# Kernel tuning notes

Hardware: AMD Instinct MI355X
Metric: run time of the kernel (lower is better)

The kernel has to match this reference:

```python
import jax, jax.numpy as jnp
import numpy as np

N, P, Q, H_DIM, HEADS, D = 4096, 128, 128, 256, 8, 64  # D = graph_dim // heads


def setup_inputs() -> dict:
    key = jax.random.key(0)
    ks = jax.random.split(key, 6)
    s = 0.05  # small scale to keep tanh/softmax in a sane range
    return {
        "x_prices": jax.random.normal(ks[0], (N, P), jnp.float32),
        "x_news": jax.random.normal(ks[1], (N, Q), jnp.float32),
        "W_bil": jax.random.normal(ks[2], (H_DIM, P, Q), jnp.float32) * s,
        "b_bil": jax.random.normal(ks[3], (H_DIM,), jnp.float32) * s,
        "Wt": jax.random.normal(ks[4], (HEADS, D, H_DIM), jnp.float32) * s,
        "a_vec": jax.random.normal(ks[5], (HEADS, 2 * D), jnp.float32) * s,
    }


def reference(x_prices, x_news, W_bil, b_bil, Wt, a_vec):
    # nn.Bilinear: out[n,h] = sum_pq x_prices[n,p] W[h,p,q] x_news[n,q] + b[h]
    x = jnp.einsum('np,hpq,nq->nh', x_prices, W_bil, x_news) + b_bil  # (N, hidden)

    # Per-head linear transform: fc_transform (no bias). Wt: (heads, d, hidden)
    xt = jnp.einsum('nh,kdh->knd', x, Wt)  # (heads, N, d)

    # Attention score a . [x_i, x_j] split into src/dst halves -> broadcast add
    d = Wt.shape[1]
    a_src, a_dst = a_vec[:, :d], a_vec[:, d:]
    s_src = jnp.einsum('knd,kd->kn', xt, a_src)  # (heads, N)
    s_dst = jnp.einsum('knd,kd->kn', xt, a_dst)  # (heads, N)
    scores = s_src[:, :, None] + s_dst[:, None, :]  # (heads, N, N)
    scores = jnp.where(scores >= 0, scores, 0.2 * scores)  # LeakyReLU(0.2)

    attn = jax.nn.softmax(scores, axis=-1)  # softmax over neighbors j
    out = jnp.einsum('knm,kmd->knd', attn, xt)  # (heads, N, d)

    # Concatenate head outputs on feature dim, then tanh
    out = jnp.transpose(out, (1, 0, 2)).reshape(xt.shape[1], -1)  # (N, heads*d)
    return jnp.tanh(out)
```

## Files before the change

kernel.cpp:

```cpp
#include <hip/hip_runtime.h>
#include <hip/hip_bf16.h>

typedef unsigned short ushort;
typedef unsigned int uint;
typedef unsigned long long u64;
typedef _Float16 f16;

#define NN 4096
#define PP 128
#define QQ 128
#define HD 256
#define KH 8
#define DD 64
#define KK 16384

typedef _Float16 f16x2 __attribute__((ext_vector_type(2)));
typedef _Float16 f16x4 __attribute__((ext_vector_type(4)));
typedef _Float16 f16x8 __attribute__((ext_vector_type(8)));
typedef __fp16 fp16x2 __attribute__((ext_vector_type(2)));
typedef float f32x4 __attribute__((ext_vector_type(4)));

__device__ inline void async_lds16(const void* g, void* l) {
  __builtin_amdgcn_global_load_lds(
      (const __attribute__((address_space(1))) unsigned int*)g,
      (__attribute__((address_space(3))) unsigned int*)l, 16, 0, 0);
}

__global__ __launch_bounds__(256) void k0_split2(
    const float* __restrict__ W, const float* __restrict__ Wt,
    f16* __restrict__ hiW, f16* __restrict__ loW,
    f16* __restrict__ hiT, f16* __restrict__ loT, float* __restrict__ xz) {
  const int tid = blockIdx.x * 256 + threadIdx.x;
  const int i = tid * 4;
  if (tid < (NN * HD) / 4)
    *(float4*)&xz[i] = make_float4(0.f, 0.f, 0.f, 0.f);
  const float* src;
  f16 *hi, *lo;
  int off;
  if (i < HD * PP * QQ) { src = W; hi = hiW; lo = loW; off = i; }
  else { src = Wt; hi = hiT; lo = loT; off = i - HD * PP * QQ; }
  const float4 w = *(const float4*)&src[off];
  const float wf[4] = {w.x, w.y, w.z, w.w};
  f16x4 hv, lv;
#pragma unroll
  for (int j = 0; j < 4; ++j) {
    const f16 h = (f16)wf[j];
    hv[j] = h;
    lv[j] = (f16)(wf[j] - (float)h);
  }
  *(f16x4*)&hi[off] = hv;
  *(f16x4*)&lo[off] = lv;
}

__global__ __launch_bounds__(256, 3) void k1_bilinear(
    const float* __restrict__ xp, const float* __restrict__ xn,
    const f16* __restrict__ Whi, const f16* __restrict__ Wlo,
    float* __restrict__ xout) {
  __shared__ f16 whi[2][128 * 32];
  __shared__ f16 wlo[2][128 * 32];
  __shared__ f16 zhi[128 * 40];
  __shared__ float xpt[8][128];

  const int t = threadIdx.x;
  const int n0 = blockIdx.x * 128;
  const int kb = blockIdx.y * (KK / 16);
  const int h0 = blockIdx.z * 128;
  const int pb = kb >> 7;

  const int l = t & 63, w = t >> 6;
  const int wr = (w >> 1) * 64, wc = (w & 1) * 64;

  int aoff[4], boff[4];
#pragma unroll
  for (int i = 0; i < 4; ++i)
    aoff[i] = (wr + i * 16 + (l & 15)) * 40 + (l >> 4) * 8;
#pragma unroll
  for (int j = 0; j < 4; ++j) {
    const int hr = wc + j * 16 + (l & 15);
    boff[j] = hr * 32 + (((l >> 4) ^ ((hr ^ (hr >> 2)) & 3)) * 8);
  }

  const int shb = t >> 2, seg = t & 3;
  int gsw[2];
#pragma unroll
  for (int g = 0; g < 2; ++g) {
    const int r = shb + 64 * g;
    gsw[g] = seg ^ ((r ^ (r >> 2)) & 3);
  }

  for (int idx = t; idx < 1024; idx += 256) {
    const int p = idx & 7, n = idx >> 3;
    xpt[p][n] = xp[(size_t)(n0 + n) * PP + pb + p];
  }

  auto stage_w = [&](int buf, int kc_) {
#pragma unroll
    for (int g = 0; g < 2; ++g) {
      const int r = shb + 64 * g;
      async_lds16(Whi + (size_t)(h0 + r) * KK + kc_ + gsw[g] * 8,
                  &whi[buf][r * 32 + seg * 8]);
      async_lds16(Wlo + (size_t)(h0 + r) * KK + kc_ + gsw[g] * 8,
                  &wlo[buf][r * 32 + seg * 8]);
    }
  };

  stage_w(0, kb);

  const int zn = t >> 1, zko = (t & 1) * 16;

  f32x4 acc[4][4];
#pragma unroll
  for (int i = 0; i < 4; ++i)
#pragma unroll
    for (int j = 0; j < 4; ++j) acc[i][j] = (f32x4)0.f;

  for (int c = 0; c < 32; ++c) {
    const int kc = kb + c * 32;
    const int pl = c >> 2;
    const int q0 = (c & 3) * 32;
    const int cur = c & 1, nxt = cur ^ 1;

    asm volatile("s_waitcnt lgkmcnt(0)" ::: "memory");
    __builtin_amdgcn_s_barrier();

    const float* xr = xn + (size_t)(n0 + zn) * QQ + q0 + zko;
    const float4 v0 = ((const float4*)xr)[0];
    const float4 v1 = ((const float4*)xr)[1];
    const float4 v2 = ((const float4*)xr)[2];
    const float4 v3 = ((const float4*)xr)[3];
    __builtin_amdgcn_sched_barrier(0);

    if (c < 31) stage_w(nxt, kc + 32);

    {
      const float xpv = xpt[pl][zn];
      float zz[16] = {v0.x, v0.y, v0.z, v0.w, v1.x, v1.y, v1.z, v1.w,
                      v2.x, v2.y, v2.z, v2.w, v3.x, v3.y, v3.z, v3.w};
      union { uint u[8]; uint4 q[2]; } ph;
#pragma unroll
      for (int j = 0; j < 8; ++j) {
        union { fp16x2 h; uint u; } cv;
        cv.h = __builtin_amdgcn_cvt_pkrtz(xpv * zz[2 * j], xpv * zz[2 * j + 1]);
        ph.u[j] = cv.u;
      }
      const int zo = zn * 40 + zko;
      *(uint4*)&zhi[zo] = ph.q[0];
      *(uint4*)&zhi[zo + 8] = ph.q[1];
    }

    if (c < 31)
      asm volatile("s_waitcnt vmcnt(4) lgkmcnt(0)" ::: "memory");
    else
      asm volatile("s_waitcnt vmcnt(0) lgkmcnt(0)" ::: "memory");
    __builtin_amdgcn_s_barrier();

    f16x8 Ah[4];
#pragma unroll
    for (int i = 0; i < 4; ++i) Ah[i] = *(const f16x8*)&zhi[aoff[i]];
#pragma unroll
    for (int j = 0; j < 4; ++j) {
      const f16x8 Bh = *(const f16x8*)&whi[cur][boff[j]];
      const f16x8 Bl = *(const f16x8*)&wlo[cur][boff[j]];
#pragma unroll
      for (int i = 0; i < 4; ++i)
        acc[i][j] = __builtin_amdgcn_mfma_f32_16x16x32_f16(Ah[i], Bh, acc[i][j], 0, 0, 0);
#pragma unroll
      for (int i = 0; i < 4; ++i)
        acc[i][j] = __builtin_amdgcn_mfma_f32_16x16x32_f16(Ah[i], Bl, acc[i][j], 0, 0, 0);
    }
  }

#pragma unroll
  for (int i = 0; i < 4; ++i)
#pragma unroll
    for (int j = 0; j < 4; ++j) {
      const int row = n0 + wr + i * 16 + (l >> 4) * 4;
      const int col = h0 + wc + j * 16 + (l & 15);
#pragma unroll
      for (int r = 0; r < 4; ++r)
        atomicAdd(&xout[(size_t)(row + r) * HD + col], acc[i][j][r]);
    }
}

__global__ __launch_bounds__(256) void k23_xt(
    const float* __restrict__ x, const float* __restrict__ bb,
    const f16* __restrict__ Wthi, const f16* __restrict__ Wtlo,
    const float* __restrict__ av, float* __restrict__ xt,
    float* __restrict__ ssrc, float* __restrict__ sdst) {
  __shared__ f16 ah[64 * 40];
  __shared__ f16 bh[128 * 32];
  __shared__ f16 bl[128 * 32];
  __shared__ float red1[2][64][17];
  __shared__ float red2[2][64][17];
  const int t = threadIdx.x;
  const int n0 = blockIdx.x * 64;
  const int c0 = blockIdx.y * 128;
  const int l = t & 63, w = t >> 6;
  const int wn = (w & 1) * 32, wcc = (w >> 1) * 64;

  int aoff[2], boff[4];
#pragma unroll
  for (int i = 0; i < 2; ++i)
    aoff[i] = (wn + i * 16 + (l & 15)) * 40 + (l >> 4) * 8;
#pragma unroll
  for (int j = 0; j < 4; ++j) {
    const int hr = wcc + j * 16 + (l & 15);
    boff[j] = hr * 32 + (((l >> 4) ^ ((hr ^ (hr >> 2)) & 3)) * 8);
  }

  f32x4 acc[2][4];
#pragma unroll
  for (int i = 0; i < 2; ++i)
#pragma unroll
    for (int j = 0; j < 4; ++j) acc[i][j] = (f32x4)0.f;

  for (int kc = 0; kc < HD; kc += 32) {
    __syncthreads();
    {
      const int row = t >> 2, sg = t & 3;
      const float* xr = &x[(size_t)(n0 + row) * HD + kc + sg * 8];
      const float4 xa = ((const float4*)xr)[0];
      const float4 xb = ((const float4*)xr)[1];
      const float4 ba = *(const float4*)&bb[kc + sg * 8];
      const float4 bv = *(const float4*)&bb[kc + sg * 8 + 4];
      f16x8 o;
      o[0] = (f16)(xa.x + ba.x); o[1] = (f16)(xa.y + ba.y);
      o[2] = (f16)(xa.z + ba.z); o[3] = (f16)(xa.w + ba.w);
      o[4] = (f16)(xb.x + bv.x); o[5] = (f16)(xb.y + bv.y);
      o[6] = (f16)(xb.z + bv.z); o[7] = (f16)(xb.w + bv.w);
      *(f16x8*)&ah[row * 40 + sg * 8] = o;
    }
#pragma unroll
    for (int g = 0; g < 2; ++g) {
      const int slot = g * 256 + t;
      const int col = slot >> 2, ps = slot & 3;
      const int ls = ps ^ ((col ^ (col >> 2)) & 3);
      *(uint4*)&bh[col * 32 + ps * 8] =
          *(const uint4*)&Wthi[(size_t)(c0 + col) * HD + kc + ls * 8];
      *(uint4*)&bl[col * 32 + ps * 8] =
          *(const uint4*)&Wtlo[(size_t)(c0 + col) * HD + kc + ls * 8];
    }
    __syncthreads();
    f16x8 Af[2];
#pragma unroll
    for (int i = 0; i < 2; ++i) Af[i] = *(const f16x8*)&ah[aoff[i]];
#pragma unroll
    for (int j = 0; j < 4; ++j) {
      const f16x8 Bh = *(const f16x8*)&bh[boff[j]];
      const f16x8 Bl = *(const f16x8*)&bl[boff[j]];
#pragma unroll
      for (int i = 0; i < 2; ++i)
        acc[i][j] = __builtin_amdgcn_mfma_f32_16x16x32_f16(Af[i], Bh, acc[i][j], 0, 0, 0);
#pragma unroll
      for (int i = 0; i < 2; ++i)
        acc[i][j] = __builtin_amdgcn_mfma_f32_16x16x32_f16(Af[i], Bl, acc[i][j], 0, 0, 0);
    }
  }

  const int hh = w >> 1;
  const int khead = (c0 >> 6) + hh;
  float a1v[4], a2v[4];
#pragma unroll
  for (int j = 0; j < 4; ++j) {
    const int d = j * 16 + (l & 15);
    a1v[j] = av[khead * (2 * DD) + d];
    a2v[j] = av[khead * (2 * DD) + DD + d];
  }

#pragma unroll
  for (int i = 0; i < 2; ++i)
#pragma unroll
    for (int r = 0; r < 4; ++r) {
      const int rowl = wn + i * 16 + (l >> 4) * 4 + r;
      float p1 = 0.f, p2 = 0.f;
#pragma unroll
      for (int j = 0; j < 4; ++j) {
        p1 += acc[i][j][r] * a1v[j];
        p2 += acc[i][j][r] * a2v[j];
      }
      red1[hh][rowl][l & 15] = p1;
      red2[hh][rowl][l & 15] = p2;
    }

#pragma unroll
  for (int i = 0; i < 2; ++i)
#pragma unroll
    for (int j = 0; j < 4; ++j) {
      const int row = n0 + wn + i * 16 + (l >> 4) * 4;
      const int colg = c0 + wcc + j * 16 + (l & 15);
      const int k = colg >> 6, d = colg & 63;
#pragma unroll
      for (int r = 0; r < 4; ++r)
        xt[((size_t)(k * NN + row + r)) * DD + d] = acc[i][j][r];
    }

  __syncthreads();
  {
    const int hh2 = t >> 7;
    const int which = (t >> 6) & 1;
    const int row = t & 63;
    const float* rp = which ? &red2[hh2][row][0] : &red1[hh2][row][0];
    float s = 0.f;
#pragma unroll
    for (int g = 0; g < 16; ++g) s += rp[g];
    const int kk = (c0 >> 6) + hh2;
    if (which) sdst[kk * NN + n0 + row] = s;
    else ssrc[kk * NN + n0 + row] = s;
  }
}

__global__ __launch_bounds__(256) void k4_rank(
    const float* __restrict__ sdst, float* __restrict__ vsorted,
    int* __restrict__ perm) {
  __shared__ u64 kv[4096];
  const int k = blockIdx.y, t = threadIdx.x;
  for (int i = t; i < 4096; i += 256) {
    const uint u = __float_as_uint(sdst[k * NN + i]);
    const uint key = (u & 0x80000000u) ? ~u : (u | 0x80000000u);
    kv[i] = ((u64)key << 32) | (uint)i;
  }
  __syncthreads();
  const int m = blockIdx.x * 256 + t;
  const u64 my = kv[m];
  int cnt = 0;
#pragma unroll 16
  for (int j = 0; j < 4096; ++j) cnt += (kv[j] < my) ? 1 : 0;
  const uint key = (uint)(my >> 32);
  const uint u = (key & 0x80000000u) ? (key ^ 0x80000000u) : ~key;
  vsorted[k * NN + cnt] = __uint_as_float(u);
  perm[k * NN + cnt] = (int)(my & 0xFFFFFFFFu);
}

__global__ __launch_bounds__(64) void k4b_chunksum(
    const float* __restrict__ vs, const int* __restrict__ perm,
    const float* __restrict__ xt, float* __restrict__ Chi, float* __restrict__ Clo) {
  __shared__ float rows[64][64];
  __shared__ float eh[64], el[64];
  const int c = blockIdx.x, k = blockIdx.y, t = threadIdx.x;
  const int base = k * NN + c * 64;
  {
    const float v = vs[base + t];
    eh[t] = __expf(v);
    el[t] = __expf(0.2f * v);
  }
#pragma unroll
  for (int r = 0; r < 16; ++r) {
    const int i = r * 4 + (t >> 4);
    const int p = perm[base + i];
    *(float4*)&rows[i][(t & 15) * 4] =
        *(const float4*)&xt[((size_t)(k * NN + p)) * DD + (t & 15) * 4];
  }
  __syncthreads();
  float shi = 0.f, slo = 0.f, whs = 0.f, wls = 0.f;
#pragma unroll 8
  for (int i = 0; i < 64; ++i) {
    const float val = rows[i][t];
    shi += eh[i] * val; slo += el[i] * val;
    whs += eh[i]; wls += el[i];
  }
  const int cb = (k * 64 + c) * 65;
  Chi[cb + t] = shi;
  Clo[cb + t] = slo;
  if (t == 0) { Chi[cb + 64] = whs; Clo[cb + 64] = wls; }
}

__global__ __launch_bounds__(64) void k4d_expand(
    const float* __restrict__ vs, const int* __restrict__ perm,
    const float* __restrict__ xt, const float* __restrict__ Chi,
    const float* __restrict__ Clo, float* __restrict__ Phi,
    float* __restrict__ Plo) {
  __shared__ float schi[64 * 65];
  __shared__ float sclo[64 * 65];
  __shared__ float rows[64][64];
  __shared__ float eh[64], el[64];
  const int c = blockIdx.x, k = blockIdx.y, t = threadIdx.x;
  const int base = k * NN + c * 64;
  for (int idx = t; idx < 4160; idx += 64) {
    schi[idx] = Chi[k * 4160 + idx];
    sclo[idx] = Clo[k * 4160 + idx];
  }
  {
    const float v = vs[base + t];
    eh[t] = __expf(v);
    el[t] = __expf(0.2f * v);
  }
#pragma unroll
  for (int r = 0; r < 16; ++r) {
    const int i = r * 4 + (t >> 4);
    const int p = perm[base + i];
    *(float4*)&rows[i][(t & 15) * 4] =
        *(const float4*)&xt[((size_t)(k * NN + p)) * DD + (t & 15) * 4];
  }
  __syncthreads();

  float run = 0.f, wrun = 0.f;
  for (int cc = 0; cc < c; ++cc) {
    run += sclo[cc * 65 + t];
    wrun += sclo[cc * 65 + 64];
  }
  float runS = 0.f, wrunS = 0.f;
  for (int cc = c + 1; cc < 64; ++cc) {
    runS += schi[cc * 65 + t];
    wrunS += schi[cc * 65 + 64];
  }

  for (int i = 0; i < 64; ++i) {
    const size_t rb = ((size_t)(k * 4097) + c * 64 + i) * 65;
    Plo[rb + t] = run;
    if (t == 0) Plo[rb + 64] = wrun;
    run += el[i] * rows[i][t];
    wrun += el[i];
  }
  if (c == 63) {
    const size_t rb = ((size_t)(k * 4097) + 4096) * 65;
    Plo[rb + t] = run;
    if (t == 0) Plo[rb + 64] = wrun;
  }
  for (int i = 63; i >= 0; --i) {
    runS += eh[i] * rows[i][t];
    wrunS += eh[i];
    const size_t rb = ((size_t)(k * 4097) + c * 64 + i) * 65;
    Phi[rb + t] = runS;
    if (t == 0) Phi[rb + 64] = wrunS;
  }
  if (c == 63) {
    const size_t rb = ((size_t)(k * 4097) + 4096) * 65;
    Phi[rb + t] = 0.f;
    if (t == 0) Phi[rb + 64] = 0.f;
  }
}

__global__ __launch_bounds__(256) void k6_final(
    const float* __restrict__ ssrc, const float* __restrict__ vsorted,
    const float* __restrict__ Phi, const float* __restrict__ Plo,
    float* __restrict__ out) {
  __shared__ float vsh[4096];
  __shared__ int posSh[16];
  const int t = threadIdx.x;
  const int q0 = blockIdx.x * 16;
  const int k = q0 >> 12;
  for (int idx = t; idx < 1024; idx += 256)
    *(float4*)&vsh[idx * 4] = *(const float4*)&vsorted[k * NN + idx * 4];
  __syncthreads();
  if (t < 16) {
    const float thr = -ssrc[q0 + t];
    int lo = 0, hi = 4096;
    while (lo < hi) {
      const int mid = (lo + hi) >> 1;
      if (vsh[mid] < thr) lo = mid + 1; else hi = mid;
    }
    posSh[t] = lo;
  }
  __syncthreads();
  const int d = t & 63;
#pragma unroll
  for (int qq = 0; qq < 4; ++qq) {
    const int ql = qq * 4 + (t >> 6);
    const int qi = q0 + ql;
    const int n = qi & 4095;
    const float u = ssrc[qi];
    const size_t rb = ((size_t)(k * 4097) + posSh[ql]) * 65;
    const float eu = __expf(u), el = __expf(0.2f * u);
    const float num = eu * Phi[rb + d] + el * Plo[rb + d];
    const float den = eu * Phi[rb + 64] + el * Plo[rb + 64];
    out[(size_t)n * (KH * DD) + k * DD + d] = tanhf(num / den);
  }
}

extern "C" void kernel_launch(void* const* d_in, const int* in_sizes, int n_in,
                              void* d_out, int out_size, void* d_ws, size_t ws_size,
                              hipStream_t stream) {
  const float* xp = (const float*)d_in[0];
  const float* xn = (const float*)d_in[1];
  const float* W = (const float*)d_in[2];
  const float* bb = (const float*)d_in[3];
  const float* Wt = (const float*)d_in[4];
  const float* av = (const float*)d_in[5];
  float* out = (float*)d_out;

  char* ws = (char*)d_ws;
  f16* Whi    = (f16*)(ws);
  f16* Wlo    = (f16*)(ws + 8388608);
  float* Phi  = (float*)(ws);
  float* Plo  = (float*)(ws + 8522240);
  float* x    = (float*)(ws + 17044480);
  float* xt   = (float*)(ws + 21238784);
  f16* Wthi   = (f16*)(ws + 31724544);
  f16* Wtlo   = (f16*)(ws + 31986688);
  float* ssrc = (float*)(ws + 32248832);
  float* sdst = (float*)(ws + 32379904);
  float* vsort= (float*)(ws + 32510976);
  int*   perm = (int*)  (ws + 32642048);
  float* Chi  = (float*)(ws + 32773120);
  float* Clo  = (float*)(ws + 32906240);

  k0_split2<<<(HD * PP * QQ + KH * DD * HD) / 1024, 256, 0, stream>>>(
      W, Wt, Whi, Wlo, Wthi, Wtlo, x);
  k1_bilinear<<<dim3(NN / 128, 16, 2), 256, 0, stream>>>(xp, xn, Whi, Wlo, x);
  k23_xt<<<dim3(NN / 64, 4), 256, 0, stream>>>(x, bb, Wthi, Wtlo, av, xt, ssrc, sdst);
  k4_rank<<<dim3(16, KH), 256, 0, stream>>>(sdst, vsort, perm);
  k4b_chunksum<<<dim3(64, KH), 64, 0, stream>>>(vsort, perm, xt, Chi, Clo);
  k4d_expand<<<dim3(64, KH), 64, 0, stream>>>(vsort, perm, xt, Chi, Clo, Phi, Plo);
  k6_final<<<(KH * NN) / 16, 256, 0, stream>>>(ssrc, vsort, Phi, Plo, out);
}
```

Before: 286.8 us.

## Form bilinear A operand in registers and swizzle blocks across XCDs

```diff
diff --git a/kernel.cpp b/kernel.cpp
--- a/kernel.cpp
+++ b/kernel.cpp
@@ -19,6 +19,8 @@
 typedef _Float16 f16x8 __attribute__((ext_vector_type(8)));
 typedef __fp16 fp16x2 __attribute__((ext_vector_type(2)));
 typedef float f32x4 __attribute__((ext_vector_type(4)));
+
+template <int N> struct IC { static constexpr int value = N; };
 
 __device__ inline void async_lds16(const void* g, void* l) {
   __builtin_amdgcn_global_load_lds(
@@ -58,22 +60,27 @@
     float* __restrict__ xout) {
   __shared__ f16 whi[2][128 * 32];
   __shared__ f16 wlo[2][128 * 32];
-  __shared__ f16 zhi[128 * 40];
   __shared__ float xpt[8][128];
 
   const int t = threadIdx.x;
-  const int n0 = blockIdx.x * 128;
-  const int kb = blockIdx.y * (KK / 16);
-  const int h0 = blockIdx.z * 128;
+  const int bid = blockIdx.x;
+  const int xcd = bid & 7, slot = bid >> 3;
+  const int jpan = slot >> 5, n_idx = slot & 31;
+  const int pan = xcd + 8 * jpan;
+  const int n0 = n_idx * 128;
+  const int kb = (pan & 15) * (KK / 16);
+  const int h0 = (pan >> 4) * 128;
   const int pb = kb >> 7;
 
   const int l = t & 63, w = t >> 6;
   const int wr = (w >> 1) * 64, wc = (w & 1) * 64;
-
-  int aoff[4], boff[4];
-#pragma unroll
-  for (int i = 0; i < 4; ++i)
-    aoff[i] = (wr + i * 16 + (l & 15)) * 40 + (l >> 4) * 8;
+  const int koff = (l >> 4) * 8;
+
+  int wrow[4];
+#pragma unroll
+  for (int i = 0; i < 4; ++i) wrow[i] = wr + i * 16 + (l & 15);
+
+  int boff[4];
 #pragma unroll
   for (int j = 0; j < 4; ++j) {
     const int hr = wc + j * 16 + (l & 15);
@@ -86,11 +93,6 @@
   for (int g = 0; g < 2; ++g) {
     const int r = shb + 64 * g;
     gsw[g] = seg ^ ((r ^ (r >> 2)) & 3);
-  }
-
-  for (int idx = t; idx < 1024; idx += 256) {
-    const int p = idx & 7, n = idx >> 3;
-    xpt[p][n] = xp[(size_t)(n0 + n) * PP + pb + p];
   }
 
   auto stage_w = [&](int buf, int kc_) {
@@ -104,70 +106,86 @@
     }
   };
 
+  f32x4 xqC[4][2];
+  auto load_xq = [&](int qidx) {
+#pragma unroll
+    for (int i = 0; i < 4; ++i) {
+      const float* p = xn + (size_t)(n0 + wrow[i]) * QQ + qidx * 32 + koff;
+      xqC[i][0] = *(const f32x4*)p;
+      xqC[i][1] = *(const f32x4*)(p + 4);
+    }
+  };
+
+  f16x8 Aa[4], Ab[4];
+  auto form_A = [&](auto NPLC, f16x8 (&AN)[4]) {
+    constexpr int npl = decltype(NPLC)::value;
+#pragma unroll
+    for (int i = 0; i < 4; ++i) {
+      const float xpv = xpt[npl][wrow[i]];
+      const f32x4 u0 = xqC[i][0], u1 = xqC[i][1];
+      union { fp16x2 h; uint u; } c0, c1, c2, c3;
+      c0.h = __builtin_amdgcn_cvt_pkrtz(xpv * u0[0], xpv * u0[1]);
+      c1.h = __builtin_amdgcn_cvt_pkrtz(xpv * u0[2], xpv * u0[3]);
+      c2.h = __builtin_amdgcn_cvt_pkrtz(xpv * u1[0], xpv * u1[1]);
+      c3.h = __builtin_amdgcn_cvt_pkrtz(xpv * u1[2], xpv * u1[3]);
+      union { uint4 u4; f16x8 f; } pk;
+      pk.u4 = make_uint4(c0.u, c1.u, c2.u, c3.u);
+      AN[i] = pk.f;
+    }
+  };
+
+  f32x4 acc[4][4];
+#pragma unroll
+  for (int i = 0; i < 4; ++i)
+#pragma unroll
+    for (int j = 0; j < 4; ++j) acc[i][j] = (f32x4)0.f;
+
+  auto stepA = [&](auto PLC, int qq, f16x8 (&AC)[4], f16x8 (&AN)[4]) {
+    constexpr int pl = decltype(PLC)::value;
+    constexpr int cb = pl & 1;
+    const bool notlast = (pl < 7) || (qq < 3);
+    if constexpr (pl == 7) {
+      if (qq < 3) load_xq(qq + 1);
+    }
+    if (notlast) {
+      constexpr int npl = (pl + 1) & 7;
+      const int nqq = (pl == 7) ? qq + 1 : qq;
+      stage_w((pl + 1) & 1, kb + npl * 128 + nqq * 32);
+    }
+#pragma unroll
+    for (int j = 0; j < 4; ++j) {
+      const f16x8 Bh = *(const f16x8*)&whi[cb][boff[j]];
+      const f16x8 Bl = *(const f16x8*)&wlo[cb][boff[j]];
+#pragma unroll
+      for (int i = 0; i < 4; ++i)
+        acc[i][j] = __builtin_amdgcn_mfma_f32_16x16x32_f16(AC[i], Bh, acc[i][j], 0, 0, 0);
+#pragma unroll
+      for (int i = 0; i < 4; ++i)
+        acc[i][j] = __builtin_amdgcn_mfma_f32_16x16x32_f16(AC[i], Bl, acc[i][j], 0, 0, 0);
+    }
+    if (notlast) form_A(IC<(pl + 1) & 7>{}, AN);
+    __syncthreads();
+  };
+
+  for (int idx = t; idx < 1024; idx += 256) {
+    const int p = idx & 7, n = idx >> 3;
+    xpt[p][n] = xp[(size_t)(n0 + n) * PP + pb + p];
+  }
+  load_xq(0);
   stage_w(0, kb);
-
-  const int zn = t >> 1, zko = (t & 1) * 16;
-
-  f32x4 acc[4][4];
-#pragma unroll
-  for (int i = 0; i < 4; ++i)
-#pragma unroll
-    for (int j = 0; j < 4; ++j) acc[i][j] = (f32x4)0.f;
-
-  for (int c = 0; c < 32; ++c) {
-    const int kc = kb + c * 32;
-    const int pl = c >> 2;
-    const int q0 = (c & 3) * 32;
-    const int cur = c & 1, nxt = cur ^ 1;
-
-    asm volatile("s_waitcnt lgkmcnt(0)" ::: "memory");
-    __builtin_amdgcn_s_barrier();
-
-    const float* xr = xn + (size_t)(n0 + zn) * QQ + q0 + zko;
-    const float4 v0 = ((const float4*)xr)[0];
-    const float4 v1 = ((const float4*)xr)[1];
-    const float4 v2 = ((const float4*)xr)[2];
-    const float4 v3 = ((const float4*)xr)[3];
-    __builtin_amdgcn_sched_barrier(0);
-
-    if (c < 31) stage_w(nxt, kc + 32);
-
-    {
-      const float xpv = xpt[pl][zn];
-      float zz[16] = {v0.x, v0.y, v0.z, v0.w, v1.x, v1.y, v1.z, v1.w,
-                      v2.x, v2.y, v2.z, v2.w, v3.x, v3.y, v3.z, v3.w};
-      union { uint u[8]; uint4 q[2]; } ph;
-#pragma unroll
-      for (int j = 0; j < 8; ++j) {
-        union { fp16x2 h; uint u; } cv;
-        cv.h = __builtin_amdgcn_cvt_pkrtz(xpv * zz[2 * j], xpv * zz[2 * j + 1]);
-        ph.u[j] = cv.u;
-      }
-      const int zo = zn * 40 + zko;
-      *(uint4*)&zhi[zo] = ph.q[0];
-      *(uint4*)&zhi[zo + 8] = ph.q[1];
-    }
-
-    if (c < 31)
-      asm volatile("s_waitcnt vmcnt(4) lgkmcnt(0)" ::: "memory");
-    else
-      asm volatile("s_waitcnt vmcnt(0) lgkmcnt(0)" ::: "memory");
-    __builtin_amdgcn_s_barrier();
-
-    f16x8 Ah[4];
-#pragma unroll
-    for (int i = 0; i < 4; ++i) Ah[i] = *(const f16x8*)&zhi[aoff[i]];
-#pragma unroll
-    for (int j = 0; j < 4; ++j) {
-      const f16x8 Bh = *(const f16x8*)&whi[cur][boff[j]];
-      const f16x8 Bl = *(const f16x8*)&wlo[cur][boff[j]];
-#pragma unroll
-      for (int i = 0; i < 4; ++i)
-        acc[i][j] = __builtin_amdgcn_mfma_f32_16x16x32_f16(Ah[i], Bh, acc[i][j], 0, 0, 0);
-#pragma unroll
-      for (int i = 0; i < 4; ++i)
-        acc[i][j] = __builtin_amdgcn_mfma_f32_16x16x32_f16(Ah[i], Bl, acc[i][j], 0, 0, 0);
-    }
+  __syncthreads();
+  form_A(IC<0>{}, Aa);
+
+#pragma unroll 1
+  for (int qq = 0; qq < 4; ++qq) {
+    stepA(IC<0>{}, qq, Aa, Ab);
+    stepA(IC<1>{}, qq, Ab, Aa);
+    stepA(IC<2>{}, qq, Aa, Ab);
+    stepA(IC<3>{}, qq, Ab, Aa);
+    stepA(IC<4>{}, qq, Aa, Ab);
+    stepA(IC<5>{}, qq, Ab, Aa);
+    stepA(IC<6>{}, qq, Aa, Ab);
+    stepA(IC<7>{}, qq, Ab, Aa);
   }
 
 #pragma unroll
@@ -496,7 +514,7 @@
 
   k0_split2<<<(HD * PP * QQ + KH * DD * HD) / 1024, 256, 0, stream>>>(
       W, Wt, Whi, Wlo, Wthi, Wtlo, x);
-  k1_bilinear<<<dim3(NN / 128, 16, 2), 256, 0, stream>>>(xp, xn, Whi, Wlo, x);
+  k1_bilinear<<<1024, 256, 0, stream>>>(xp, xn, Whi, Wlo, x);
   k23_xt<<<dim3(NN / 64, 4), 256, 0, stream>>>(x, bb, Wthi, Wtlo, av, xt, ssrc, sdst);
   k4_rank<<<dim3(16, KH), 256, 0, stream>>>(sdst, vsort, perm);
   k4b_chunksum<<<dim3(64, KH), 64, 0, stream>>>(vsort, perm, xt, Chi, Clo);
```

Result: slower. 325.4 us (+13.5%).
